# Optimization experiments

Hardware: AMD Instinct MI355X
Metric: run time of the kernel (lower is better)

## Reference

```python
import jax, jax.numpy as jnp
import numpy as np

N = 50000          # nodes
E = 800000         # edges
IN_NODE = 256      # in_node_feats
IN_EDGE = 32       # in_edge_feats (reward broadcast dim)
H = 4              # num_heads
O = 64             # out_node_feats
NEG_SLOPE = 0.2    # dgl default leaky_relu negative slope


def setup_inputs() -> dict:
    key = jax.random.key(0)
    ks = jax.random.split(key, 10)
    s = 0.05
    return {
        "nfeats": jax.random.normal(ks[0], (N, IN_NODE), jnp.float32),
        "reward": jax.random.uniform(ks[1], (E,), jnp.float32),
        "src": jax.random.randint(ks[2], (E,), 0, N, jnp.int32),
        "dst": jax.random.randint(ks[3], (E,), 0, N, jnp.int32),
        "W_ni": jax.random.normal(ks[4], (IN_NODE, H * O), jnp.float32) * s,
        "W_nj": jax.random.normal(ks[5], (IN_NODE, H * O), jnp.float32) * s,
        "W_fij": jax.random.normal(ks[6], (IN_EDGE, H * O), jnp.float32) * s,
        "W_node": jax.random.normal(ks[7], (IN_NODE, H * O), jnp.float32) * s,
        "bias": jax.random.normal(ks[8], (H * O,), jnp.float32) * s,
        "attn": jax.random.normal(ks[9], (H, O), jnp.float32) * s,
    }


def reference(nfeats, reward, src, dst, W_ni, W_nj, W_fij, W_node, bias, attn):
    # efeats: scalar reward broadcast to IN_EDGE features per edge
    efeats = jnp.repeat(reward[:, None], IN_EDGE, axis=1)            # [E, Fe]
    # EdgeGATConv attention logits
    f_ni = nfeats @ W_ni                                             # [N, H*O]
    f_nj = nfeats @ W_nj                                             # [N, H*O]
    f_fij = efeats @ W_fij                                           # [E, H*O]
    f = f_ni[src] + f_nj[dst] + f_fij + bias                         # [E, H*O]
    f = jax.nn.leaky_relu(f, NEG_SLOPE).reshape(E, H, O)
    e = jnp.einsum("eho,ho->eh", f, attn)                            # [E, H]
    # edge softmax over incoming edges per destination node
    emax = jax.lax.stop_gradient(jax.ops.segment_max(e, dst, num_segments=N))
    ee = jnp.exp(e - emax[dst])                                      # [E, H]
    denom = jax.ops.segment_sum(ee, dst, num_segments=N)             # [N, H]
    a = ee / denom[dst]                                              # [E, H]
    # weighted scatter-sum aggregation of projected source features
    h_src = (nfeats @ W_node).reshape(N, H, O)
    m = h_src[src] * a[:, :, None]                                   # [E, H, O]
    h_out = jax.ops.segment_sum(m, dst, num_segments=N)              # [N, H, O]
    # wrapper: mean over heads then ReLU
    return jax.nn.relu(h_out.mean(-2))                               # [N, O]
```

## Files before the change

kernel.cpp:

```cpp
#include <hip/hip_runtime.h>


typedef unsigned short ushort_t;
typedef __attribute__((ext_vector_type(8))) short frag_t;
typedef __attribute__((ext_vector_type(4))) float f32x4;
typedef unsigned long long u64_t;

#define CSTRIDE 16

__device__ __forceinline__ ushort_t f2bf(float f) {
    unsigned u = __float_as_uint(f);
    unsigned r = u + 0x7fffu + ((u >> 16) & 1u);
    return (ushort_t)(r >> 16);
}
__device__ __forceinline__ float bf2f(ushort_t v) {
    return __uint_as_float(((unsigned)v) << 16);
}
__device__ __forceinline__ float2 bfx2(unsigned u) {
    float2 f;
    f.x = __uint_as_float(u << 16);
    f.y = __uint_as_float(u & 0xffff0000u);
    return f;
}

template <int CTRL>
__device__ __forceinline__ float dpp_add(float v) {
    int s = __builtin_amdgcn_update_dpp(0, __float_as_int(v), CTRL, 0xF, 0xF, true);
    return v + __int_as_float(s);
}

__device__ __forceinline__ void async_load16(const void* g, void* l) {
    __builtin_amdgcn_global_load_lds(
        (const __attribute__((address_space(1))) unsigned int*)g,
        (__attribute__((address_space(3))) unsigned int*)(unsigned int)(uintptr_t)l,
        16, 0, 0);
}

__global__ __launch_bounds__(256) void prep_kernel(
    const float* __restrict__ nfeats, const float* __restrict__ Wni,
    const float* __restrict__ Wnj, const float* __restrict__ Wnode,
    const float* __restrict__ Wfij, const int* __restrict__ dst,
    ushort_t* __restrict__ Abf, ushort_t* __restrict__ BcatT,
    float* __restrict__ wsum, int* __restrict__ counts,
    int* __restrict__ posArr,
    int castB, int countB, int total4, int E) {
    int b = blockIdx.x;
    int t = threadIdx.x;
    if (b < castB) {
#pragma unroll
        for (int cc = 0; cc < 4; ++cc) {
            int i = (b * 4 + cc) * 256 + t;
            if (i >= total4) break;
            float4 v = *(const float4*)(nfeats + (size_t)i * 4);
            ushort4 o;
            o.x = f2bf(v.x); o.y = f2bf(v.y); o.z = f2bf(v.z); o.w = f2bf(v.w);
            *(ushort4*)(Abf + (size_t)i * 4) = o;
        }
    } else if (b < castB + 768) {
        int j = b - castB;
        int seg = j >> 8;
        const float* W = (seg == 0) ? Wni : (seg == 1) ? Wnj : Wnode;
        BcatT[(size_t)j * 256 + t] = f2bf(W[(size_t)t * 256 + (j & 255)]);
    } else if (b < castB + 768 + countB) {
        int i = (b - castB - 768) * 256 + t;
        if (i < E)
            posArr[i] = atomicAdd(&counts[(size_t)dst[i] * CSTRIDE], 1);
    } else {
        float s = 0.f;
#pragma unroll
        for (int k = 0; k < 32; ++k) s += Wfij[k * 256 + t];
        wsum[t] = s;
    }
}


__global__ __launch_bounds__(256) void scan_block_sums(const int* __restrict__ counts,
                                                       int* __restrict__ bsum, int N) {
    __shared__ int sm[256];
    int i = blockIdx.x * 256 + threadIdx.x;
    sm[threadIdx.x] = (i < N) ? counts[(size_t)i * CSTRIDE] : 0;
    __syncthreads();
#pragma unroll
    for (int off = 128; off; off >>= 1) {
        if (threadIdx.x < off) sm[threadIdx.x] += sm[threadIdx.x + off];
        __syncthreads();
    }
    if (threadIdx.x == 0) bsum[blockIdx.x] = sm[0];
}

__global__ __launch_bounds__(256) void scan_final(const int* __restrict__ counts,
                                                  const int* __restrict__ bsum,
                                                  int* __restrict__ rowptr,
                                                  int N, int E) {
    __shared__ int sm[256];
    __shared__ int smp[256];
    int t = threadIdx.x;
    int b = blockIdx.x;
    int i = b * 256 + t;

    smp[t] = (t < b) ? bsum[t] : 0;
    int c = (i < N) ? counts[(size_t)i * CSTRIDE] : 0;
    sm[t] = c;
    __syncthreads();
#pragma unroll
    for (int off = 128; off; off >>= 1) {
        if (t < off) smp[t] += smp[t + off];
        __syncthreads();
    }
    int prefix = smp[0];
    for (int off = 1; off < 256; off <<= 1) {
        int v = (t >= off) ? sm[t - off] : 0;
        __syncthreads();
        sm[t] += v;
        __syncthreads();
    }
    int ex = prefix + sm[t] - c;
    if (i < N) rowptr[i] = ex;
    if (i == 0) rowptr[N] = E;
}

__global__ __launch_bounds__(256) void sg_fused(
    const int* __restrict__ src, const int* __restrict__ dst,
    const float* __restrict__ reward, const int* __restrict__ rowptr,
    const int* __restrict__ posArr, u64_t* __restrict__ epair, int E, int gemmB,
    const ushort_t* __restrict__ A, const ushort_t* __restrict__ BT,
    const float* __restrict__ bias, ushort_t* __restrict__ fni,
    ushort_t* __restrict__ fhv, ushort_t* __restrict__ fnj, int N, int gX) {
    __shared__ ushort_t As[2][128][32];
    __shared__ ushort_t Bs[2][128][32];

    if ((int)blockIdx.x >= gemmB) {
        int i = ((int)blockIdx.x - gemmB) * 256 + threadIdx.x;
        if (i < E) {
            int d = dst[i];
            int pos = rowptr[d] + posArr[i];
            epair[pos] = ((u64_t)__float_as_uint(reward[i]) << 32) | (unsigned)src[i];
        }
        return;
    }

    const int bx = blockIdx.x;
    const int brow = bx % gX;
    const int bcol = bx / gX;

    const int tid = threadIdx.x;
    const int wave = tid >> 6, lane = tid & 63;
    const int quad = lane >> 4, l16 = lane & 15;
    const int wr = wave & 1, wc = wave >> 1;
    const int row0 = brow * 128;
    const int col0 = bcol * 128;
    const int Nm1 = N - 1;
    const int srow = lane >> 2;
    const int skof = (lane & 3) * 8;

    f32x4 acc[4][4] = {};

#pragma unroll
    for (int j = 0; j < 2; ++j) {
        int r = wave * 32 + j * 16 + srow;
        int grow = row0 + r; if (grow > Nm1) grow = Nm1;
        async_load16(A + (size_t)grow * 256 + skof, &As[0][wave * 32 + j * 16][0]);
        async_load16(BT + (size_t)(col0 + r) * 256 + skof, &Bs[0][wave * 32 + j * 16][0]);
    }

    for (int it = 0; it < 8; ++it) {
        const int cur = it & 1;
        __syncthreads();
        if (it < 7) {
            const int k1 = (it + 1) * 32;
#pragma unroll
            for (int j = 0; j < 2; ++j) {
                int r = wave * 32 + j * 16 + srow;
                int grow = row0 + r; if (grow > Nm1) grow = Nm1;
                async_load16(A + (size_t)grow * 256 + k1 + skof,
                             &As[1 - cur][wave * 32 + j * 16][0]);
                async_load16(BT + (size_t)(col0 + r) * 256 + k1 + skof,
                             &Bs[1 - cur][wave * 32 + j * 16][0]);
            }
        }

        frag_t af[4], bfr[4];
#pragma unroll
        for (int i = 0; i < 4; ++i)
            af[i] = *(const frag_t*)&As[cur][wr * 64 + i * 16 + l16][quad * 8];
#pragma unroll
        for (int j = 0; j < 4; ++j)
            bfr[j] = *(const frag_t*)&Bs[cur][wc * 64 + j * 16 + l16][quad * 8];

#pragma unroll
        for (int i = 0; i < 4; ++i)
#pragma unroll
            for (int j = 0; j < 4; ++j)
                acc[i][j] = __builtin_amdgcn_mfma_f32_16x16x32_bf16(af[i], bfr[j], acc[i][j], 0, 0, 0);
    }

#pragma unroll
    for (int i = 0; i < 4; ++i) {
#pragma unroll
        for (int j = 0; j < 4; ++j) {
#pragma unroll
            for (int r = 0; r < 4; ++r) {
                int row = row0 + wr * 64 + i * 16 + quad * 4 + r;
                if (row >= N) continue;
                int col = col0 + wc * 64 + j * 16 + l16;
                float v = acc[i][j][r];
                if (col < 256) {
                    fni[(size_t)row * 256 + col] = f2bf(v + bias[col]);
                } else if (col < 512) {
                    fnj[(size_t)row * 256 + (col - 256)] = f2bf(v);
                } else {
                    int c2 = col - 512;
                    int h = c2 >> 6, o = c2 & 63;
                    fhv[(size_t)row * 256 + ((h * 16 + (o & 15)) << 2) + (o >> 4)] =
                        f2bf(v);
                }
            }
        }
    }
}


__global__ __launch_bounds__(256) void node_fused(
    const ushort_t* __restrict__ fni, const ushort_t* __restrict__ fhv,
    const ushort_t* __restrict__ fnj,
    const int* __restrict__ rowptr, const u64_t* __restrict__ epair,
    const float* __restrict__ wsum, const float* __restrict__ attn,
    float* __restrict__ out, int N) {
    int node = (int)((blockIdx.x * (size_t)blockDim.x + threadIdx.x) >> 6);
    int lane = threadIdx.x & 63;
    if (node >= N) return;

    const int base = __builtin_amdgcn_readfirstlane(rowptr[node]);
    const int end = __builtin_amdgcn_readfirstlane(rowptr[node + 1]);
    const int j0 = lane * 4;
    if (base >= end) { out[(size_t)node * 64 + lane] = 0.f; return; }

    float4 ws = *(const float4*)(wsum + j0);
    float4 at = *(const float4*)(attn + j0);
    const float L2E = 1.44269504088896f;
    at.x *= L2E; at.y *= L2E; at.z *= L2E; at.w *= L2E;
    ushort4 njv = *(const ushort4*)(fnj + (size_t)node * 256 + j0);
    float nj0 = bf2f(njv.x), nj1 = bf2f(njv.y), nj2 = bf2f(njv.z), nj3 = bf2f(njv.w);

    float a0 = 0.f, a1 = 0.f, a2 = 0.f, a3 = 0.f, dsum = 0.f;
    const int last = end - 1;

    auto prow = [&](const ushort_t* tbl, u64_t p) -> uint2 {
        unsigned s = (unsigned)p;
        return *(const uint2*)(tbl + (size_t)s * 256 + j0);
    };

    auto edge = [&](u64_t p, uint2 ni, uint2 hv, bool live) {
        float r = __uint_as_float((unsigned)(p >> 32));
        float2 b01 = bfx2(ni.x), b23 = bfx2(ni.y);
        float x0 = fmaf(r, ws.x, nj0) + b01.x;
        float x1 = fmaf(r, ws.y, nj1) + b01.y;
        float x2 = fmaf(r, ws.z, nj2) + b23.x;
        float x3 = fmaf(r, ws.w, nj3) + b23.y;
        x0 = fmaxf(x0, 0.2f * x0);
        x1 = fmaxf(x1, 0.2f * x1);
        x2 = fmaxf(x2, 0.2f * x2);
        x3 = fmaxf(x3, 0.2f * x3);
        float acc = at.x * x0 + at.y * x1 + at.z * x2 + at.w * x3;
        acc = dpp_add<0xB1>(acc);
        acc = dpp_add<0x4E>(acc);
        acc = dpp_add<0x124>(acc);
        acc = dpp_add<0x128>(acc);
        float eh = live ? exp2f(acc) : 0.f;
        dsum += eh;
        float2 h01 = bfx2(hv.x), h23 = bfx2(hv.y);
        a0 = fmaf(eh, h01.x, a0);
        a1 = fmaf(eh, h01.y, a1);
        a2 = fmaf(eh, h23.x, a2);
        a3 = fmaf(eh, h23.y, a3);
    };

    u64_t p0 = epair[base];
    u64_t p1 = epair[min(base + 1, last)];
    u64_t p2 = epair[min(base + 2, last)];
    u64_t p3 = epair[min(base + 3, last)];
    u64_t p4 = epair[min(base + 4, last)];
    u64_t p5 = epair[min(base + 5, last)];

    uint2 niA = prow(fni, p0), hvA = prow(fhv, p0);
    uint2 niB = prow(fni, p1), hvB = prow(fhv, p1);
    uint2 niC = prow(fni, p2), hvC = prow(fhv, p2);
    uint2 niD = prow(fni, p3), hvD = prow(fhv, p3);

    for (int e = base; e < end; e += 2) {
        uint2 niE = prow(fni, p4), hvE = prow(fhv, p4);
        uint2 niF = prow(fni, p5), hvF = prow(fhv, p5);
        u64_t p6 = epair[min(e + 6, last)];
        u64_t p7 = epair[min(e + 7, last)];

        edge(p0, niA, hvA, true);
        edge(p1, niB, hvB, e + 1 <= last);

        p0 = p2; p1 = p3; p2 = p4; p3 = p5; p4 = p6; p5 = p7;
        niA = niC; hvA = hvC; niB = niD; hvB = hvD;
        niC = niE; hvC = hvE; niD = niF; hvD = hvF;
    }

    float inv = __fdividef(0.25f, dsum);
    float v0 = a0 * inv, v1 = a1 * inv, v2 = a2 * inv, v3 = a3 * inv;
    v0 += __shfl_xor(v0, 16, 64); v1 += __shfl_xor(v1, 16, 64);
    v2 += __shfl_xor(v2, 16, 64); v3 += __shfl_xor(v3, 16, 64);
    v0 += __shfl_xor(v0, 32, 64); v1 += __shfl_xor(v1, 32, 64);
    v2 += __shfl_xor(v2, 32, 64); v3 += __shfl_xor(v3, 32, 64);
    int quad = lane >> 4;
    float v = (quad == 0) ? v0 : (quad == 1) ? v1 : (quad == 2) ? v2 : v3;
    out[(size_t)node * 64 + lane] = fmaxf(v, 0.f);
}


extern "C" void kernel_launch(void* const* d_in, const int* in_sizes, int n_in,
                              void* d_out, int out_size, void* d_ws, size_t ws_size,
                              hipStream_t stream) {
    const float* nfeats = (const float*)d_in[0];
    const float* reward = (const float*)d_in[1];
    const int* src = (const int*)d_in[2];
    const int* dst = (const int*)d_in[3];
    const float* Wni = (const float*)d_in[4];
    const float* Wnj = (const float*)d_in[5];
    const float* Wfij = (const float*)d_in[6];
    const float* Wnode = (const float*)d_in[7];
    const float* bias = (const float*)d_in[8];
    const float* attn = (const float*)d_in[9];
    float* out = (float*)d_out;

    const int N = in_sizes[0] / 256;
    const int E = in_sizes[1];
    const int NB = (N + 255) / 256;
    const int total4 = N * 64;
    const int castB = (total4 + 1023) / 1024;
    const int countB = (E + 255) / 256;

    char* p = (char*)d_ws;
    auto alloc = [&](size_t bytes) { char* r = p; p += (bytes + 63) & ~63ull; return r; };
    u64_t* epair = (u64_t*)alloc((size_t)E * sizeof(u64_t));
    float* wsum = (float*)alloc(256 * sizeof(float));
    int* counts = (int*)alloc((size_t)N * CSTRIDE * sizeof(int));
    int* bsum = (int*)alloc(256 * sizeof(int));
    int* rowptr = (int*)alloc((size_t)(N + 1) * sizeof(int));
    int* posArr = (int*)alloc((size_t)E * sizeof(int));
    ushort_t* fni = (ushort_t*)alloc((size_t)N * 256 * sizeof(ushort_t));
    ushort_t* fhv = (ushort_t*)alloc((size_t)N * 256 * sizeof(ushort_t));
    ushort_t* fnj = (ushort_t*)alloc((size_t)N * 256 * sizeof(ushort_t));
    ushort_t* Abf = (ushort_t*)alloc((size_t)N * 256 * sizeof(ushort_t));
    ushort_t* BcatT = (ushort_t*)alloc((size_t)768 * 256 * sizeof(ushort_t));

    (void)hipMemsetAsync(counts, 0, (size_t)N * CSTRIDE * sizeof(int), stream);

    prep_kernel<<<castB + 768 + countB + 1, 256, 0, stream>>>(
        nfeats, Wni, Wnj, Wnode, Wfij, dst, Abf, BcatT, wsum, counts, posArr,
        castB, countB, total4, E);

    scan_block_sums<<<NB, 256, 0, stream>>>(counts, bsum, N);
    scan_final<<<NB, 256, 0, stream>>>(counts, bsum, rowptr, N, E);

    const int gX = (N + 127) / 128;
    const int gemmB = gX * 6;
    sg_fused<<<gemmB + countB, 256, 0, stream>>>(
        src, dst, reward, rowptr, posArr, epair, E, gemmB,
        Abf, BcatT, bias, fni, fhv, fnj, N, gX);

    node_fused<<<(N + 3) / 4, 256, 0, stream>>>(fni, fhv, fnj, rowptr, epair,
                                                wsum, attn, out, N);
}
```

Measured before the change: 321.8 us.

## Keep full 64-row A panel in LDS and sweep all output columns per block

The GEMM in sg_fused switches from 128x128 output tiles, which reloaded A for each of 6 column tiles, to 64-row blocks. Each block loads its whole 64x256 A panel into LDS once and loops over all 768 output columns, double-buffering only the B tiles. This is meant to cut redundant global reads of A and spread the work over more, smaller blocks. In exchange, each block now runs a long serial loop, per-wave MFMA work per B tile is smaller, and B is reread by every block.

```diff
diff --git a/kernel.cpp b/kernel.cpp
--- a/kernel.cpp
+++ b/kernel.cpp
@@ -126,7 +126,7 @@
     const ushort_t* __restrict__ A, const ushort_t* __restrict__ BT,
     const float* __restrict__ bias, ushort_t* __restrict__ fni,
     ushort_t* __restrict__ fhv, ushort_t* __restrict__ fnj, int N, int gX) {
-    __shared__ ushort_t As[2][128][32];
+    __shared__ ushort_t Afull[8][64][32];
     __shared__ ushort_t Bs[2][128][32];
 
     if ((int)blockIdx.x >= gemmB) {
@@ -139,81 +139,83 @@
         return;
     }
 
-    const int bx = blockIdx.x;
-    const int brow = bx % gX;
-    const int bcol = bx / gX;
-
+    const int row0 = (int)blockIdx.x * 64;
     const int tid = threadIdx.x;
     const int wave = tid >> 6, lane = tid & 63;
     const int quad = lane >> 4, l16 = lane & 15;
-    const int wr = wave & 1, wc = wave >> 1;
-    const int row0 = brow * 128;
-    const int col0 = bcol * 128;
     const int Nm1 = N - 1;
     const int srow = lane >> 2;
     const int skof = (lane & 3) * 8;
 
-    f32x4 acc[4][4] = {};
-
-#pragma unroll
-    for (int j = 0; j < 2; ++j) {
-        int r = wave * 32 + j * 16 + srow;
-        int grow = row0 + r; if (grow > Nm1) grow = Nm1;
-        async_load16(A + (size_t)grow * 256 + skof, &As[0][wave * 32 + j * 16][0]);
-        async_load16(BT + (size_t)(col0 + r) * 256 + skof, &Bs[0][wave * 32 + j * 16][0]);
-    }
-
-    for (int it = 0; it < 8; ++it) {
-        const int cur = it & 1;
-        __syncthreads();
-        if (it < 7) {
-            const int k1 = (it + 1) * 32;
+    {
+        int rL = wave * 16 + (lane >> 2);
+        int grow = row0 + rL; if (grow > Nm1) grow = Nm1;
+        const ushort_t* gsrc = A + (size_t)grow * 256 + (lane & 3) * 8;
+#pragma unroll
+        for (int i = 0; i < 8; ++i)
+            async_load16(gsrc + i * 32, &Afull[i][wave * 16][0]);
+    }
+
+    auto stageB = [&](int buf, int colbase, int kof) {
+#pragma unroll
+        for (int j = 0; j < 2; ++j) {
+            int rr = wave * 32 + j * 16 + srow;
+            async_load16(BT + (size_t)(colbase + rr) * 256 + kof + skof,
+                         &Bs[buf][wave * 32 + j * 16][0]);
+        }
+    };
+    stageB(0, 0, 0);
+
+    f32x4 acc[4][2] = {};
+
+    for (int col = 0; col < 6; ++col) {
+        const int colb = col * 128;
+#pragma unroll
+        for (int it = 0; it < 8; ++it) {
+            const int g = col * 8 + it;
+            const int cur = g & 1;
+            __syncthreads();
+            if (g < 47) {
+                const int gn = g + 1;
+                stageB(1 - cur, (gn >> 3) * 128, (gn & 7) * 32);
+            }
+            frag_t af[4], bfr[2];
+#pragma unroll
+            for (int i = 0; i < 4; ++i)
+                af[i] = *(const frag_t*)&Afull[it][i * 16 + l16][quad * 8];
+#pragma unroll
+            for (int j = 0; j < 2; ++j)
+                bfr[j] = *(const frag_t*)&Bs[cur][wave * 32 + j * 16 + l16][quad * 8];
+#pragma unroll
+            for (int i = 0; i < 4; ++i)
+#pragma unroll
+                for (int j = 0; j < 2; ++j)
+                    acc[i][j] = __builtin_amdgcn_mfma_f32_16x16x32_bf16(
+                        af[i], bfr[j], acc[i][j], 0, 0, 0);
+        }
+
+#pragma unroll
+        for (int i = 0; i < 4; ++i) {
 #pragma unroll
             for (int j = 0; j < 2; ++j) {
-                int r = wave * 32 + j * 16 + srow;
-                int grow = row0 + r; if (grow > Nm1) grow = Nm1;
-                async_load16(A + (size_t)grow * 256 + k1 + skof,
-                             &As[1 - cur][wave * 32 + j * 16][0]);
-                async_load16(BT + (size_t)(col0 + r) * 256 + k1 + skof,
-                             &Bs[1 - cur][wave * 32 + j * 16][0]);
-            }
-        }
-
-        frag_t af[4], bfr[4];
-#pragma unroll
-        for (int i = 0; i < 4; ++i)
-            af[i] = *(const frag_t*)&As[cur][wr * 64 + i * 16 + l16][quad * 8];
-#pragma unroll
-        for (int j = 0; j < 4; ++j)
-            bfr[j] = *(const frag_t*)&Bs[cur][wc * 64 + j * 16 + l16][quad * 8];
-
-#pragma unroll
-        for (int i = 0; i < 4; ++i)
-#pragma unroll
-            for (int j = 0; j < 4; ++j)
-                acc[i][j] = __builtin_amdgcn_mfma_f32_16x16x32_bf16(af[i], bfr[j], acc[i][j], 0, 0, 0);
-    }
-
-#pragma unroll
-    for (int i = 0; i < 4; ++i) {
-#pragma unroll
-        for (int j = 0; j < 4; ++j) {
-#pragma unroll
-            for (int r = 0; r < 4; ++r) {
-                int row = row0 + wr * 64 + i * 16 + quad * 4 + r;
-                if (row >= N) continue;
-                int col = col0 + wc * 64 + j * 16 + l16;
-                float v = acc[i][j][r];
-                if (col < 256) {
-                    fni[(size_t)row * 256 + col] = f2bf(v + bias[col]);
-                } else if (col < 512) {
-                    fnj[(size_t)row * 256 + (col - 256)] = f2bf(v);
-                } else {
-                    int c2 = col - 512;
-                    int h = c2 >> 6, o = c2 & 63;
-                    fhv[(size_t)row * 256 + ((h * 16 + (o & 15)) << 2) + (o >> 4)] =
-                        f2bf(v);
+#pragma unroll
+                for (int rr = 0; rr < 4; ++rr) {
+                    int row = row0 + i * 16 + quad * 4 + rr;
+                    if (row >= N) continue;
+                    int cg = colb + wave * 32 + j * 16 + l16;
+                    float v = acc[i][j][rr];
+                    if (cg < 256) {
+                        fni[(size_t)row * 256 + cg] = f2bf(v + bias[cg]);
+                    } else if (cg < 512) {
+                        fnj[(size_t)row * 256 + (cg - 256)] = f2bf(v);
+                    } else {
+                        int c2 = cg - 512;
+                        int h = c2 >> 6, o = c2 & 63;
+                        fhv[(size_t)row * 256 + ((h * 16 + (o & 15)) << 2) + (o >> 4)] =
+                            f2bf(v);
+                    }
                 }
+                acc[i][j] = (f32x4){0.f, 0.f, 0.f, 0.f};
             }
         }
     }
@@ -358,10 +360,9 @@
     scan_block_sums<<<NB, 256, 0, stream>>>(counts, bsum, N);
     scan_final<<<NB, 256, 0, stream>>>(counts, bsum, rowptr, N, E);
 
-    const int gX = (N + 127) / 128;
-    const int gemmB = gX * 6;
-    sg_fused<<<gemmB + countB, 256, 0, stream>>>(
-        src, dst, reward, rowptr, posArr, epair, E, gemmB,
+    const int gX = (N + 63) / 64;
+    sg_fused<<<gX + countB, 256, 0, stream>>>(
+        src, dst, reward, rowptr, posArr, epair, E, gX,
         Abf, BcatT, bias, fni, fhv, fnj, N, gX);
 
     node_fused<<<(N + 3) / 4, 256, 0, stream>>>(fni, fhv, fnj, rowptr, epair,
```

New measurement: 339.4 us. +5.5%, slower.

## Split each node's edge list across two waves and combine via shared memory

Applied to the files above, without the earlier changes.

Each destination node is now handled by two wavefronts, each processing half of its incoming edges. The two partial softmax-weighted sums are then merged through LDS after a block barrier. The edge prefetch is also deepened: the index pipeline now holds eight epair entries and rotates through register sets without copying. This is meant to expose more memory-level parallelism and shorten the per-node serial gather chain. The cost is twice as many waves, a __syncthreads per block, and one wave per node that idles during finalisation.

```diff
diff --git a/kernel.cpp b/kernel.cpp
--- a/kernel.cpp
+++ b/kernel.cpp
@@ -226,90 +226,124 @@
     const int* __restrict__ rowptr, const u64_t* __restrict__ epair,
     const float* __restrict__ wsum, const float* __restrict__ attn,
     float* __restrict__ out, int N) {
-    int node = (int)((blockIdx.x * (size_t)blockDim.x + threadIdx.x) >> 6);
-    int lane = threadIdx.x & 63;
-    if (node >= N) return;
-
-    const int base = __builtin_amdgcn_readfirstlane(rowptr[node]);
-    const int end = __builtin_amdgcn_readfirstlane(rowptr[node + 1]);
+    __shared__ float comb[5][4][64];
+
+    const int wave = threadIdx.x >> 6;
+    const int lane = threadIdx.x & 63;
+    const int nodeIdx = (int)blockIdx.x * 2 + (wave >> 1);
+    const int half = wave & 1;
+    const bool valid = nodeIdx < N;
+    const int nodeC = valid ? nodeIdx : 0;
+
+    const int nbase = __builtin_amdgcn_readfirstlane(rowptr[nodeC]);
+    const int nend = __builtin_amdgcn_readfirstlane(rowptr[nodeC + 1]);
+    const int deg = nend - nbase;
+    const int mid = nbase + ((deg + 1) >> 1);
+    int base = half ? mid : nbase;
+    int end = half ? nend : mid;
+    if (!valid) { base = 0; end = 0; }
+
     const int j0 = lane * 4;
-    if (base >= end) { out[(size_t)node * 64 + lane] = 0.f; return; }
-
-    float4 ws = *(const float4*)(wsum + j0);
-    float4 at = *(const float4*)(attn + j0);
-    const float L2E = 1.44269504088896f;
-    at.x *= L2E; at.y *= L2E; at.z *= L2E; at.w *= L2E;
-    ushort4 njv = *(const ushort4*)(fnj + (size_t)node * 256 + j0);
-    float nj0 = bf2f(njv.x), nj1 = bf2f(njv.y), nj2 = bf2f(njv.z), nj3 = bf2f(njv.w);
-
     float a0 = 0.f, a1 = 0.f, a2 = 0.f, a3 = 0.f, dsum = 0.f;
-    const int last = end - 1;
-
-    auto prow = [&](const ushort_t* tbl, u64_t p) -> uint2 {
-        unsigned s = (unsigned)p;
-        return *(const uint2*)(tbl + (size_t)s * 256 + j0);
-    };
-
-    auto edge = [&](u64_t p, uint2 ni, uint2 hv, bool live) {
-        float r = __uint_as_float((unsigned)(p >> 32));
-        float2 b01 = bfx2(ni.x), b23 = bfx2(ni.y);
-        float x0 = fmaf(r, ws.x, nj0) + b01.x;
-        float x1 = fmaf(r, ws.y, nj1) + b01.y;
-        float x2 = fmaf(r, ws.z, nj2) + b23.x;
-        float x3 = fmaf(r, ws.w, nj3) + b23.y;
-        x0 = fmaxf(x0, 0.2f * x0);
-        x1 = fmaxf(x1, 0.2f * x1);
-        x2 = fmaxf(x2, 0.2f * x2);
-        x3 = fmaxf(x3, 0.2f * x3);
-        float acc = at.x * x0 + at.y * x1 + at.z * x2 + at.w * x3;
-        acc = dpp_add<0xB1>(acc);
-        acc = dpp_add<0x4E>(acc);
-        acc = dpp_add<0x124>(acc);
-        acc = dpp_add<0x128>(acc);
-        float eh = live ? exp2f(acc) : 0.f;
-        dsum += eh;
-        float2 h01 = bfx2(hv.x), h23 = bfx2(hv.y);
-        a0 = fmaf(eh, h01.x, a0);
-        a1 = fmaf(eh, h01.y, a1);
-        a2 = fmaf(eh, h23.x, a2);
-        a3 = fmaf(eh, h23.y, a3);
-    };
-
-    u64_t p0 = epair[base];
-    u64_t p1 = epair[min(base + 1, last)];
-    u64_t p2 = epair[min(base + 2, last)];
-    u64_t p3 = epair[min(base + 3, last)];
-    u64_t p4 = epair[min(base + 4, last)];
-    u64_t p5 = epair[min(base + 5, last)];
-
-    uint2 niA = prow(fni, p0), hvA = prow(fhv, p0);
-    uint2 niB = prow(fni, p1), hvB = prow(fhv, p1);
-    uint2 niC = prow(fni, p2), hvC = prow(fhv, p2);
-    uint2 niD = prow(fni, p3), hvD = prow(fhv, p3);
-
-    for (int e = base; e < end; e += 2) {
-        uint2 niE = prow(fni, p4), hvE = prow(fhv, p4);
-        uint2 niF = prow(fni, p5), hvF = prow(fhv, p5);
-        u64_t p6 = epair[min(e + 6, last)];
-        u64_t p7 = epair[min(e + 7, last)];
-
-        edge(p0, niA, hvA, true);
-        edge(p1, niB, hvB, e + 1 <= last);
-
-        p0 = p2; p1 = p3; p2 = p4; p3 = p5; p4 = p6; p5 = p7;
-        niA = niC; hvA = hvC; niB = niD; hvB = hvD;
-        niC = niE; hvC = hvE; niD = niF; hvD = hvF;
-    }
-
-    float inv = __fdividef(0.25f, dsum);
-    float v0 = a0 * inv, v1 = a1 * inv, v2 = a2 * inv, v3 = a3 * inv;
-    v0 += __shfl_xor(v0, 16, 64); v1 += __shfl_xor(v1, 16, 64);
-    v2 += __shfl_xor(v2, 16, 64); v3 += __shfl_xor(v3, 16, 64);
-    v0 += __shfl_xor(v0, 32, 64); v1 += __shfl_xor(v1, 32, 64);
-    v2 += __shfl_xor(v2, 32, 64); v3 += __shfl_xor(v3, 32, 64);
-    int quad = lane >> 4;
-    float v = (quad == 0) ? v0 : (quad == 1) ? v1 : (quad == 2) ? v2 : v3;
-    out[(size_t)node * 64 + lane] = fmaxf(v, 0.f);
+
+    if (base < end) {
+        float4 ws = *(const float4*)(wsum + j0);
+        float4 at = *(const float4*)(attn + j0);
+        const float L2E = 1.44269504088896f;
+        at.x *= L2E; at.y *= L2E; at.z *= L2E; at.w *= L2E;
+        ushort4 njv = *(const ushort4*)(fnj + (size_t)nodeC * 256 + j0);
+        float nj0 = bf2f(njv.x), nj1 = bf2f(njv.y), nj2 = bf2f(njv.z), nj3 = bf2f(njv.w);
+
+        const int last = end - 1;
+        int e = base;
+
+        auto prow = [&](const ushort_t* tbl, u64_t p) -> uint2 {
+            unsigned s = (unsigned)p;
+            return *(const uint2*)(tbl + (size_t)s * 256 + j0);
+        };
+        auto proc = [&](u64_t p, uint2 ni, uint2 hv, bool live) {
+            float r = __uint_as_float((unsigned)(p >> 32));
+            float2 b01 = bfx2(ni.x), b23 = bfx2(ni.y);
+            float x0 = fmaf(r, ws.x, nj0) + b01.x;
+            float x1 = fmaf(r, ws.y, nj1) + b01.y;
+            float x2 = fmaf(r, ws.z, nj2) + b23.x;
+            float x3 = fmaf(r, ws.w, nj3) + b23.y;
+            x0 = fmaxf(x0, 0.2f * x0);
+            x1 = fmaxf(x1, 0.2f * x1);
+            x2 = fmaxf(x2, 0.2f * x2);
+            x3 = fmaxf(x3, 0.2f * x3);
+            float acc = at.x * x0 + at.y * x1 + at.z * x2 + at.w * x3;
+            acc = dpp_add<0xB1>(acc);
+            acc = dpp_add<0x4E>(acc);
+            acc = dpp_add<0x124>(acc);
+            acc = dpp_add<0x128>(acc);
+            float eh = live ? exp2f(acc) : 0.f;
+            dsum += eh;
+            float2 h01 = bfx2(hv.x), h23 = bfx2(hv.y);
+            a0 = fmaf(eh, h01.x, a0);
+            a1 = fmaf(eh, h01.y, a1);
+            a2 = fmaf(eh, h23.x, a2);
+            a3 = fmaf(eh, h23.y, a3);
+        };
+
+        u64_t P0 = epair[e];
+        u64_t P1 = epair[min(e + 1, last)];
+        u64_t P2 = epair[min(e + 2, last)];
+        u64_t P3 = epair[min(e + 3, last)];
+        u64_t P4 = epair[min(e + 4, last)];
+        u64_t P5 = epair[min(e + 5, last)];
+        u64_t P6 = epair[min(e + 6, last)];
+        u64_t P7 = epair[min(e + 7, last)];
+        uint2 nA = prow(fni, P0), hA = prow(fhv, P0);
+        uint2 nB = prow(fni, P1), hB = prow(fhv, P1);
+        uint2 nC = prow(fni, P2), hC = prow(fhv, P2);
+        uint2 nD = prow(fni, P3), hD = prow(fhv, P3);
+
+        auto halfstep = [&](u64_t& Pa, u64_t& Pb, u64_t Pc, u64_t Pd,
+                            uint2& nX, uint2& hX, uint2& nY, uint2& hY) -> bool {
+            proc(Pa, nX, hX, true);
+            proc(Pb, nY, hY, e + 1 <= last);
+            nX = prow(fni, Pc); hX = prow(fhv, Pc);
+            nY = prow(fni, Pd); hY = prow(fhv, Pd);
+            Pa = epair[min(e + 8, last)];
+            Pb = epair[min(e + 9, last)];
+            e += 2;
+            return e < end;
+        };
+
+        for (;;) {
+            if (!halfstep(P0, P1, P4, P5, nA, hA, nB, hB)) break;
+            if (!halfstep(P2, P3, P6, P7, nC, hC, nD, hD)) break;
+            if (!halfstep(P4, P5, P0, P1, nA, hA, nB, hB)) break;
+            if (!halfstep(P6, P7, P2, P3, nC, hC, nD, hD)) break;
+        }
+    }
+
+    comb[0][wave][lane] = a0;
+    comb[1][wave][lane] = a1;
+    comb[2][wave][lane] = a2;
+    comb[3][wave][lane] = a3;
+    comb[4][wave][lane] = dsum;
+    __syncthreads();
+
+    if (half == 0 && valid) {
+        const int pw = wave ^ 1;
+        a0 += comb[0][pw][lane];
+        a1 += comb[1][pw][lane];
+        a2 += comb[2][pw][lane];
+        a3 += comb[3][pw][lane];
+        dsum += comb[4][pw][lane];
+
+        float inv = dsum > 0.f ? __fdividef(0.25f, dsum) : 0.f;
+        float v0 = a0 * inv, v1 = a1 * inv, v2 = a2 * inv, v3 = a3 * inv;
+        v0 += __shfl_xor(v0, 16, 64); v1 += __shfl_xor(v1, 16, 64);
+        v2 += __shfl_xor(v2, 16, 64); v3 += __shfl_xor(v3, 16, 64);
+        v0 += __shfl_xor(v0, 32, 64); v1 += __shfl_xor(v1, 32, 64);
+        v2 += __shfl_xor(v2, 32, 64); v3 += __shfl_xor(v3, 32, 64);
+        int quad = lane >> 4;
+        float v = (quad == 0) ? v0 : (quad == 1) ? v1 : (quad == 2) ? v2 : v3;
+        out[(size_t)nodeIdx * 64 + lane] = fmaxf(v, 0.f);
+    }
 }
 
 
@@ -364,6 +398,6 @@
         src, dst, reward, rowptr, posArr, epair, E, gemmB,
         Abf, BcatT, bias, fni, fhv, fnj, N, gX);
 
-    node_fused<<<(N + 3) / 4, 256, 0, stream>>>(fni, fhv, fnj, rowptr, epair,
+    node_fused<<<(N + 1) / 2, 256, 0, stream>>>(fni, fhv, fnj, rowptr, epair,
                                                 wsum, attn, out, N);
 }
```

Result: slower. 335.0 us (+4.1%).
